# Kernel optimization log

Hardware: AMD Instinct MI355X
Metric: run time of the kernel (lower is better)

Reference implementation:

```python
import jax, jax.numpy as jnp
import numpy as np

HEADS = 8
DIM_HEAD = 64
SCALE = DIM_HEAD ** -0.5


def setup_inputs() -> dict:
    key = jax.random.key(0)
    ks = jax.random.split(key, 6)
    B, N, D = 4, 2048, 512
    inner = HEADS * DIM_HEAD  # 512
    x = jax.random.normal(ks[0], (B, N, D), dtype=jnp.float32)
    centroid_delta = jax.random.normal(ks[1], (B, 3, N, N), dtype=jnp.float32)
    Wqkv = jax.random.normal(ks[2], (D, 3 * inner), dtype=jnp.float32) * (D ** -0.5)
    Wout = jax.random.normal(ks[3], (inner, D), dtype=jnp.float32) * (inner ** -0.5)
    bout = jnp.zeros((D,), dtype=jnp.float32)
    rel_w = jax.random.normal(ks[4], (HEADS, 3), dtype=jnp.float32)
    rel_b = jnp.zeros((HEADS,), dtype=jnp.float32)
    return {"x": x, "centroid_delta": centroid_delta, "Wqkv": Wqkv,
            "Wout": Wout, "bout": bout, "rel_w": rel_w, "rel_b": rel_b}


def reference(x, centroid_delta, Wqkv, Wout, bout, rel_w, rel_b):
    B, N, D = x.shape
    h, d = HEADS, DIM_HEAD
    qkv = x @ Wqkv                      # [B, N, 3*h*d]
    q, k, v = jnp.split(qkv, 3, axis=-1)
    # [B, N, h*d] -> [B, h, N, d]
    reshape = lambda t: t.reshape(B, N, h, d).transpose(0, 2, 1, 3)
    q, k, v = reshape(q), reshape(k), reshape(v)
    dots = jnp.einsum('bhid,bhjd->bhij', q, k) * SCALE  # [B, h, N, N]
    # 1x1 conv: Conv2d(3, heads, 1) on centroid_delta [B, 3, N, N]
    bias = jnp.einsum('hc,bcij->bhij', rel_w, centroid_delta) + rel_b[None, :, None, None]
    attn = jax.nn.softmax(dots + bias, axis=-1)
    out = jnp.einsum('bhij,bhjd->bhid', attn, v)        # [B, h, N, d]
    out = out.transpose(0, 2, 1, 3).reshape(B, N, h * d)
    return out @ Wout + bout
```

## Files before the change

### kernel.cpp

```cpp
#include <hip/hip_runtime.h>
#include <hip/hip_bf16.h>
#include <hip/hip_fp16.h>

typedef __bf16 bf16_t;
typedef __bf16 bf16x8 __attribute__((ext_vector_type(8)));
typedef float f32x4 __attribute__((ext_vector_type(4)));

#define SCALE_ 0.125f
#define BATCH 4
#define NSEQ 2048
#define DMODEL 512
#define HEADS 8
#define DHEAD 64
#define QKVN 1536
#define NN ((size_t)NSEQ * NSEQ)

#define BAR() asm volatile("s_waitcnt lgkmcnt(0)\n\ts_barrier" ::: "memory")

__device__ __forceinline__ void gload_lds16(const void* g, void* l) {
  __builtin_amdgcn_global_load_lds((const __attribute__((address_space(1))) void*)g,
                                   (__attribute__((address_space(3))) void*)l, 16, 0, 0);
}

__device__ __forceinline__ f32x4 mfma16(bf16x8 a, bf16x8 b, f32x4 c) {
  return __builtin_amdgcn_mfma_f32_16x16x32_bf16(a, b, c, 0, 0, 0);
}

__device__ __forceinline__ int pkmax_f16(int a, int b) {
  int d;
  asm("v_pk_max_f16 %0, %1, %2" : "=v"(d) : "v"(a), "v"(b));
  return d;
}

template<int CTRL>
__device__ __forceinline__ int movdpp(int x) {
  return __builtin_amdgcn_update_dpp(0, x, CTRL, 0xf, 0xf, true);
}

__global__ __launch_bounds__(256) void cvt_bf16_kernel(const float* __restrict__ in,
                                                       bf16_t* __restrict__ out, int n4) {
  int i = blockIdx.x * 256 + threadIdx.x;
  if (i < n4) {
    float4 v = ((const float4*)in)[i];
    union { bf16_t b[4]; uint2 u; } pk;
    pk.b[0] = (bf16_t)v.x; pk.b[1] = (bf16_t)v.y;
    pk.b[2] = (bf16_t)v.z; pk.b[3] = (bf16_t)v.w;
    ((uint2*)out)[i] = pk.u;
  }
}

__global__ __launch_bounds__(256) void cvt_transpose_kernel(const float* __restrict__ in,
                                                            bf16_t* __restrict__ out, int R, int C) {
  __shared__ float tile[64][65];
  const int r0 = blockIdx.y * 64, c0 = blockIdx.x * 64;
  const int tx = threadIdx.x & 63, tg = threadIdx.x >> 6;
#pragma unroll
  for (int i = 0; i < 16; i++) {
    int rr = tg * 16 + i;
    tile[rr][tx] = in[(size_t)(r0 + rr) * C + c0 + tx];
  }
  __syncthreads();
#pragma unroll
  for (int i = 0; i < 16; i++) {
    int cc = tg * 16 + i;
    out[(size_t)(c0 + cc) * R + r0 + tx] = (bf16_t)tile[tx][cc];
  }
}

template<int BIAS, int OUTF32, int VSPLIT>
__global__ __launch_bounds__(256) void gemm128_kernel(const bf16_t* __restrict__ A,
    const bf16_t* __restrict__ Bt, void* __restrict__ Cout,
    const float* __restrict__ bias, bf16_t* __restrict__ vt, int M, int N, int K) {
  __shared__ __align__(16) bf16_t SM[2][128 * 64];
  bf16_t* As = SM[0];
  bf16_t* Bs = SM[1];
  const int tid = threadIdx.x;
  const int w = tid >> 6, lane = tid & 63, quad = lane >> 4, l16 = lane & 15;
  const int wm = w & 1, wn = w >> 1;
  const int m0 = blockIdx.x * 128, n0 = blockIdx.y * 128;
  f32x4 acc[4][4] = {};
  int srow[4], scg[4];
#pragma unroll
  for (int t = 0; t < 4; t++) {
    int s = (w * 4 + t) * 64 + lane;
    srow[t] = s >> 3;
    scg[t] = (s & 7) ^ (srow[t] & 7);
  }
  for (int k0 = 0; k0 < K; k0 += 64) {
#pragma unroll
    for (int t = 0; t < 4; t++) {
      gload_lds16(&A[(size_t)(m0 + srow[t]) * K + k0 + scg[t] * 8], &As[(w * 4 + t) * 512]);
      gload_lds16(&Bt[(size_t)(n0 + srow[t]) * K + k0 + scg[t] * 8], &Bs[(w * 4 + t) * 512]);
    }
    __syncthreads();
    bf16x8 af[4][2], bfr[4][2];
#pragma unroll
    for (int mt = 0; mt < 4; mt++) {
      int row = wm * 64 + mt * 16 + l16;
#pragma unroll
      for (int kh = 0; kh < 2; kh++)
        af[mt][kh] = *(const bf16x8*)&As[(row * 8 + ((kh * 4 + quad) ^ (row & 7))) * 8];
    }
#pragma unroll
    for (int nt = 0; nt < 4; nt++) {
      int row = wn * 64 + nt * 16 + l16;
#pragma unroll
      for (int kh = 0; kh < 2; kh++)
        bfr[nt][kh] = *(const bf16x8*)&Bs[(row * 8 + ((kh * 4 + quad) ^ (row & 7))) * 8];
    }
#pragma unroll
    for (int mt = 0; mt < 4; mt++)
#pragma unroll
      for (int nt = 0; nt < 4; nt++) {
        acc[mt][nt] = mfma16(af[mt][0], bfr[nt][0], acc[mt][nt]);
        acc[mt][nt] = mfma16(af[mt][1], bfr[nt][1], acc[mt][nt]);
      }
    __syncthreads();
  }
  if (VSPLIT && n0 >= 1024) {
    bf16_t* T = &SM[0][0];
#pragma unroll
    for (int nt = 0; nt < 4; nt++) {
      int hdl = wn * 64 + nt * 16 + l16;
#pragma unroll
      for (int mt = 0; mt < 4; mt++) {
        int nloc = wm * 64 + mt * 16 + quad * 4;
        union { bf16_t e[4]; uint2 u; } pk;
#pragma unroll
        for (int rr = 0; rr < 4; rr++) pk.e[rr] = (bf16_t)acc[mt][nt][rr];
        *(uint2*)&T[hdl * 128 + nloc] = pk.u;
      }
    }
    __syncthreads();
    const int bb = m0 >> 11, nn0 = m0 & 2047;
#pragma unroll
    for (int pass = 0; pass < 2; pass++) {
      const int r = pass * 64 + (tid >> 2);
      const size_t gb = ((size_t)(bb * 512 + (n0 - 1024) + r)) * NSEQ + nn0;
#pragma unroll
      for (int i = 0; i < 4; i++) {
        int c = i * 32 + (tid & 3) * 8;
        *(uint4*)&vt[gb + c] = *(const uint4*)&T[r * 128 + c];
      }
    }
    return;
  }
#pragma unroll
  for (int nt = 0; nt < 4; nt++) {
    int col = n0 + wn * 64 + nt * 16 + l16;
    float bv = BIAS ? bias[col] : 0.0f;
#pragma unroll
    for (int mt = 0; mt < 4; mt++) {
#pragma unroll
      for (int rr = 0; rr < 4; rr++) {
        int row = m0 + wm * 64 + mt * 16 + quad * 4 + rr;
        float v = acc[mt][nt][rr] + bv;
        if (OUTF32) ((float*)Cout)[(size_t)row * N + col] = v;
        else        ((bf16_t*)Cout)[(size_t)row * N + col] = (bf16_t)v;
      }
    }
  }
}

__global__ __launch_bounds__(256, 4) void attn_kernel(const bf16_t* __restrict__ qkv,
    const bf16_t* __restrict__ vt,
    const float* __restrict__ cd, const float* __restrict__ rel_w,
    const float* __restrict__ rel_b, bf16_t* __restrict__ ao) {
  __shared__ __align__(16) bf16_t Ks[64][72];
  __shared__ __align__(16) bf16_t Vts[64][72];
  __shared__ __align__(16) bf16_t Ps[64][72];
  const int tid = threadIdx.x;
  const int w = tid >> 6, lane = tid & 63, quad = lane >> 4, l16 = lane & 15;
  const int bid = blockIdx.x;
  const int h = bid >> 7, b = (bid >> 5) & 3, it = bid & 31;

  const size_t qoff = (size_t)(b * NSEQ + it * 64 + w * 16 + l16) * QKVN + h * DHEAD;
  bf16x8 q0 = *(const bf16x8*)&qkv[qoff + quad * 8];
  bf16x8 q1 = *(const bf16x8*)&qkv[qoff + 32 + quad * 8];

  const float rw0 = rel_w[h * 3 + 0], rw1 = rel_w[h * 3 + 1], rw2 = rel_w[h * 3 + 2];
  const float rb = rel_b[h];

  bf16x8 ones;
#pragma unroll
  for (int e = 0; e < 8; e++) ones[e] = (bf16_t)1.0f;

  f32x4 o[4] = {};
  float m_r[4], l_r[4];
#pragma unroll
  for (int r = 0; r < 4; r++) { m_r[r] = -1e30f; l_r[r] = 0.0f; }

  const int sr = tid >> 3, sg = tid & 7;
  const size_t kbase = (size_t)b * NSEQ * QKVN + DMODEL + h * DHEAD;
  const size_t vtb = (size_t)(b * HEADS + h) * 64 * NSEQ;
  const int vc0 = (sg ^ ((sr >> 3) & 3)) * 8;

  const int row0 = it * 64 + w * 16 + quad * 4;
  const float* cdp = cd + (size_t)b * 3 * NN + (size_t)row0 * NSEQ + l16;
  float biasr[4][4];
#define LOADBIAS(JT) do { const int jb_ = (JT) * 64;                                   \
  _Pragma("unroll") for (int ct_ = 0; ct_ < 4; ct_++)                                  \
  _Pragma("unroll") for (int r_ = 0; r_ < 4; r_++) {                                   \
    size_t ci_ = (size_t)r_ * NSEQ + jb_ + ct_ * 16;                                   \
    biasr[ct_][r_] = fmaf(rw0, cdp[ci_],                                               \
                     fmaf(rw1, cdp[ci_ + NN], fmaf(rw2, cdp[ci_ + 2 * NN], rb)));      \
  } } while (0)

  uint4 k0r, k1r, v0r, v1r;
  {
    const bf16_t* p = &qkv[kbase + (size_t)sr * QKVN + sg * 8];
    k0r = *(const uint4*)p;
    k1r = *(const uint4*)(p + 32 * QKVN);
    const bf16_t* pv = &vt[vtb + (size_t)sr * NSEQ + sg * 8];
    v0r = *(const uint4*)pv;
    v1r = *(const uint4*)(pv + 32 * NSEQ);
  }
  LOADBIAS(0);

  for (int jt = 0; jt < 32; jt++) {
    *(uint4*)&Ks[sr][sg * 8]      = k0r;
    *(uint4*)&Ks[sr + 32][sg * 8] = k1r;
    *(uint4*)&Vts[sr][vc0]        = v0r;
    *(uint4*)&Vts[sr + 32][vc0]   = v1r;
    BAR();

    if (jt < 31) {
      const bf16_t* p = &qkv[kbase + (size_t)((jt + 1) * 64 + sr) * QKVN + sg * 8];
      k0r = *(const uint4*)p;
      k1r = *(const uint4*)(p + 32 * QKVN);
      const bf16_t* pv = &vt[vtb + (size_t)sr * NSEQ + (jt + 1) * 64 + sg * 8];
      v0r = *(const uint4*)pv;
      v1r = *(const uint4*)(pv + 32 * NSEQ);
    }

    f32x4 s[4] = {};
#pragma unroll
    for (int ct = 0; ct < 4; ct++) {
      bf16x8 b0 = *(const bf16x8*)&Ks[ct * 16 + l16][quad * 8];
      bf16x8 b1 = *(const bf16x8*)&Ks[ct * 16 + l16][32 + quad * 8];
      s[ct] = mfma16(q0, b0, s[ct]);
      s[ct] = mfma16(q1, b1, s[ct]);
    }

#pragma unroll
    for (int ct = 0; ct < 4; ct++)
#pragma unroll
      for (int r = 0; r < 4; r++)
        s[ct][r] = s[ct][r] * SCALE_ + biasr[ct][r];
    if (jt < 31) LOADBIAS(jt + 1);

    float mx[4];
#pragma unroll
    for (int r = 0; r < 4; r++)
      mx[r] = fmaxf(fmaxf(s[0][r], s[1][r]), fmaxf(s[2][r], s[3][r]));
    {
      union { __half h[2]; int i; } u01, u23;
      u01.h[0] = __float2half(mx[0]); u01.h[1] = __float2half(mx[1]);
      u23.h[0] = __float2half(mx[2]); u23.h[1] = __float2half(mx[3]);
      u01.i = pkmax_f16(u01.i, movdpp<0x128>(u01.i));
      u23.i = pkmax_f16(u23.i, movdpp<0x128>(u23.i));
      u01.i = pkmax_f16(u01.i, movdpp<0x124>(u01.i));
      u23.i = pkmax_f16(u23.i, movdpp<0x124>(u23.i));
      u01.i = pkmax_f16(u01.i, movdpp<0x122>(u01.i));
      u23.i = pkmax_f16(u23.i, movdpp<0x122>(u23.i));
      u01.i = pkmax_f16(u01.i, movdpp<0x121>(u01.i));
      u23.i = pkmax_f16(u23.i, movdpp<0x121>(u23.i));
      mx[0] = __half2float(u01.h[0]); mx[1] = __half2float(u01.h[1]);
      mx[2] = __half2float(u23.h[0]); mx[3] = __half2float(u23.h[1]);
    }
    float alpha[4];
#pragma unroll
    for (int r = 0; r < 4; r++) {
      float mnew = fmaxf(m_r[r], mx[r]);
      alpha[r] = __expf(m_r[r] - mnew);
      m_r[r] = mnew;
#pragma unroll
      for (int ct = 0; ct < 4; ct++)
        s[ct][r] = __expf(s[ct][r] - mnew);
#pragma unroll
      for (int dt = 0; dt < 4; dt++) o[dt][r] *= alpha[r];
    }

#pragma unroll
    for (int ct = 0; ct < 4; ct++)
#pragma unroll
      for (int rr = 0; rr < 4; rr++)
        Ps[w * 16 + quad * 4 + rr][(ct * 16 + l16) ^ (quad << 3)] = (bf16_t)s[ct][rr];

    const int psw = ((l16 >> 2) & 3) << 3;
    bf16x8 p0 = *(const bf16x8*)&Ps[w * 16 + l16][(quad * 8) ^ psw];
    bf16x8 p1 = *(const bf16x8*)&Ps[w * 16 + l16][32 + ((quad * 8) ^ psw)];
#pragma unroll
    for (int dt = 0; dt < 4; dt++) {
      const int row = dt * 16 + l16;
      const int vsw = ((row >> 3) & 3) << 3;
      bf16x8 v0 = *(const bf16x8*)&Vts[row][(quad * 8) ^ vsw];
      bf16x8 v1 = *(const bf16x8*)&Vts[row][32 + ((quad * 8) ^ vsw)];
      o[dt] = mfma16(p0, v0, o[dt]);
      o[dt] = mfma16(p1, v1, o[dt]);
    }
    {
      f32x4 ls = {};
      ls = mfma16(p0, ones, ls);
      ls = mfma16(p1, ones, ls);
#pragma unroll
      for (int r = 0; r < 4; r++) l_r[r] = l_r[r] * alpha[r] + ls[r];
    }
    BAR();
  }

#pragma unroll
  for (int dt = 0; dt < 4; dt++) {
    int col = h * DHEAD + dt * 16 + l16;
#pragma unroll
    for (int rr = 0; rr < 4; rr++) {
      int row = b * NSEQ + it * 64 + w * 16 + quad * 4 + rr;
      ao[(size_t)row * DMODEL + col] = (bf16_t)(o[dt][rr] / l_r[rr]);
    }
  }
#undef LOADBIAS
}

extern "C" void kernel_launch(void* const* d_in, const int* in_sizes, int n_in,
                              void* d_out, int out_size, void* d_ws, size_t ws_size,
                              hipStream_t stream) {
  const float* x     = (const float*)d_in[0];
  const float* cd    = (const float*)d_in[1];
  const float* Wqkv  = (const float*)d_in[2];
  const float* Wout  = (const float*)d_in[3];
  const float* bout  = (const float*)d_in[4];
  const float* rel_w = (const float*)d_in[5];
  const float* rel_b = (const float*)d_in[6];
  float* out = (float*)d_out;

  char* ws = (char*)d_ws;
  const size_t M = (size_t)BATCH * NSEQ;
  bf16_t* xb    = (bf16_t*)ws;
  bf16_t* WqkvT = (bf16_t*)(ws + 8388608);
  bf16_t* WoutT = (bf16_t*)(ws + 8388608 + 1572864);
  bf16_t* qkv   = (bf16_t*)(ws + 8388608 + 1572864 + 524288);
  bf16_t* ao    = (bf16_t*)(ws + 8388608 + 1572864 + 524288 + 25165824);
  bf16_t* vtw   = (bf16_t*)(ws + 8388608 + 1572864 + 524288 + 25165824 + 8388608);

  cvt_bf16_kernel<<<(int)(M * DMODEL / 4 / 256), 256, 0, stream>>>(x, xb, (int)(M * DMODEL / 4));
  cvt_transpose_kernel<<<dim3(QKVN / 64, DMODEL / 64), 256, 0, stream>>>(Wqkv, WqkvT, DMODEL, QKVN);
  cvt_transpose_kernel<<<dim3(DMODEL / 64, DMODEL / 64), 256, 0, stream>>>(Wout, WoutT, DMODEL, DMODEL);

  gemm128_kernel<0, 0, 1><<<dim3(M / 128, QKVN / 128), 256, 0, stream>>>(
      xb, WqkvT, (void*)qkv, nullptr, vtw, (int)M, QKVN, DMODEL);

  attn_kernel<<<BATCH * 32 * HEADS, 256, 0, stream>>>(qkv, vtw, cd, rel_w, rel_b, ao);

  gemm128_kernel<1, 1, 0><<<dim3(M / 128, DMODEL / 128), 256, 0, stream>>>(
      ao, WoutT, (void*)out, bout, nullptr, (int)M, DMODEL, DMODEL);
}
```

Before: 454.0 us.

## Split attention over two key halves and merge partial softmax results

Each attention block now processes half of the key sequence, doubling the grid so more blocks run concurrently across compute units. Unnormalized fp32 partial outputs plus per-row max and sum are written to workspace. A new merge kernel combines the two halves with log-sum-exp rescaling and writes bf16 output. This adds extra global traffic for the partials and one more kernel launch.

```diff
diff --git a/kernel.cpp b/kernel.cpp
--- a/kernel.cpp
+++ b/kernel.cpp
@@ -165,14 +165,17 @@
 __global__ __launch_bounds__(256, 4) void attn_kernel(const bf16_t* __restrict__ qkv,
     const bf16_t* __restrict__ vt,
     const float* __restrict__ cd, const float* __restrict__ rel_w,
-    const float* __restrict__ rel_b, bf16_t* __restrict__ ao) {
+    const float* __restrict__ rel_b, float* __restrict__ opart,
+    float2* __restrict__ mls) {
   __shared__ __align__(16) bf16_t Ks[64][72];
   __shared__ __align__(16) bf16_t Vts[64][72];
   __shared__ __align__(16) bf16_t Ps[64][72];
   const int tid = threadIdx.x;
   const int w = tid >> 6, lane = tid & 63, quad = lane >> 4, l16 = lane & 15;
   const int bid = blockIdx.x;
-  const int h = bid >> 7, b = (bid >> 5) & 3, it = bid & 31;
+  const int hj = bid >> 7, h = hj >> 1, jh = hj & 1;
+  const int b = (bid >> 5) & 3, it = bid & 31;
+  const int jbase = jh * 1024;
 
   const size_t qoff = (size_t)(b * NSEQ + it * 64 + w * 16 + l16) * QKVN + h * DHEAD;
   bf16x8 q0 = *(const bf16x8*)&qkv[qoff + quad * 8];
@@ -198,7 +201,7 @@
   const int row0 = it * 64 + w * 16 + quad * 4;
   const float* cdp = cd + (size_t)b * 3 * NN + (size_t)row0 * NSEQ + l16;
   float biasr[4][4];
-#define LOADBIAS(JT) do { const int jb_ = (JT) * 64;                                   \
+#define LOADBIAS(JTA) do { const int jb_ = (JTA) * 64;                                 \
   _Pragma("unroll") for (int ct_ = 0; ct_ < 4; ct_++)                                  \
   _Pragma("unroll") for (int r_ = 0; r_ < 4; r_++) {                                   \
     size_t ci_ = (size_t)r_ * NSEQ + jb_ + ct_ * 16;                                   \
@@ -208,27 +211,27 @@
 
   uint4 k0r, k1r, v0r, v1r;
   {
-    const bf16_t* p = &qkv[kbase + (size_t)sr * QKVN + sg * 8];
+    const bf16_t* p = &qkv[kbase + (size_t)(jbase + sr) * QKVN + sg * 8];
     k0r = *(const uint4*)p;
     k1r = *(const uint4*)(p + 32 * QKVN);
-    const bf16_t* pv = &vt[vtb + (size_t)sr * NSEQ + sg * 8];
+    const bf16_t* pv = &vt[vtb + (size_t)sr * NSEQ + jbase + sg * 8];
     v0r = *(const uint4*)pv;
     v1r = *(const uint4*)(pv + 32 * NSEQ);
   }
-  LOADBIAS(0);
-
-  for (int jt = 0; jt < 32; jt++) {
+  LOADBIAS(jh * 16);
+
+  for (int jt = 0; jt < 16; jt++) {
     *(uint4*)&Ks[sr][sg * 8]      = k0r;
     *(uint4*)&Ks[sr + 32][sg * 8] = k1r;
     *(uint4*)&Vts[sr][vc0]        = v0r;
     *(uint4*)&Vts[sr + 32][vc0]   = v1r;
     BAR();
 
-    if (jt < 31) {
-      const bf16_t* p = &qkv[kbase + (size_t)((jt + 1) * 64 + sr) * QKVN + sg * 8];
+    if (jt < 15) {
+      const bf16_t* p = &qkv[kbase + (size_t)(jbase + (jt + 1) * 64 + sr) * QKVN + sg * 8];
       k0r = *(const uint4*)p;
       k1r = *(const uint4*)(p + 32 * QKVN);
-      const bf16_t* pv = &vt[vtb + (size_t)sr * NSEQ + (jt + 1) * 64 + sg * 8];
+      const bf16_t* pv = &vt[vtb + (size_t)sr * NSEQ + jbase + (jt + 1) * 64 + sg * 8];
       v0r = *(const uint4*)pv;
       v1r = *(const uint4*)(pv + 32 * NSEQ);
     }
@@ -247,7 +250,7 @@
 #pragma unroll
       for (int r = 0; r < 4; r++)
         s[ct][r] = s[ct][r] * SCALE_ + biasr[ct][r];
-    if (jt < 31) LOADBIAS(jt + 1);
+    if (jt < 15) LOADBIAS(jh * 16 + jt + 1);
 
     float mx[4];
 #pragma unroll
@@ -309,16 +312,47 @@
     BAR();
   }
 
+  float* ob = opart + (size_t)bid * 4096;
 #pragma unroll
   for (int dt = 0; dt < 4; dt++) {
-    int col = h * DHEAD + dt * 16 + l16;
+    int col = dt * 16 + l16;
 #pragma unroll
     for (int rr = 0; rr < 4; rr++) {
-      int row = b * NSEQ + it * 64 + w * 16 + quad * 4 + rr;
-      ao[(size_t)row * DMODEL + col] = (bf16_t)(o[dt][rr] / l_r[rr]);
+      int rl = w * 16 + quad * 4 + rr;
+      ob[rl * 64 + col] = o[dt][rr];
+    }
+  }
+  if (l16 == 0) {
+#pragma unroll
+    for (int r = 0; r < 4; r++) {
+      int rl = w * 16 + quad * 4 + r;
+      mls[(size_t)bid * 64 + rl] = make_float2(m_r[r], l_r[r]);
     }
   }
 #undef LOADBIAS
+}
+
+__global__ __launch_bounds__(256) void merge_kernel(const float* __restrict__ opart,
+    const float2* __restrict__ mls, bf16_t* __restrict__ ao) {
+  int qi = blockIdx.x * 256 + threadIdx.x;
+  int gr = qi >> 7;
+  int c4 = (qi & 127) << 2;
+  int h = c4 >> 6, d = c4 & 63;
+  int b = gr >> 11, n = gr & 2047, it = n >> 6, rl = n & 63;
+  int bid0 = h * 256 + b * 32 + it;
+  int bid1 = bid0 + 128;
+  float2 s0 = mls[(size_t)bid0 * 64 + rl];
+  float2 s1 = mls[(size_t)bid1 * 64 + rl];
+  float m = fmaxf(s0.x, s1.x);
+  float e0 = __expf(s0.x - m), e1 = __expf(s1.x - m);
+  float rinv = 1.0f / (s0.y * e0 + s1.y * e1);
+  f32x4 o0 = *(const f32x4*)&opart[(size_t)bid0 * 4096 + rl * 64 + d];
+  f32x4 o1 = *(const f32x4*)&opart[(size_t)bid1 * 4096 + rl * 64 + d];
+  union { bf16_t e[4]; uint2 u; } pk;
+#pragma unroll
+  for (int i = 0; i < 4; i++)
+    pk.e[i] = (bf16_t)((o0[i] * e0 + o1[i] * e1) * rinv);
+  *(uint2*)&ao[(size_t)gr * DMODEL + c4] = pk.u;
 }
 
 extern "C" void kernel_launch(void* const* d_in, const int* in_sizes, int n_in,
@@ -338,9 +372,11 @@
   bf16_t* xb    = (bf16_t*)ws;
   bf16_t* WqkvT = (bf16_t*)(ws + 8388608);
   bf16_t* WoutT = (bf16_t*)(ws + 8388608 + 1572864);
-  bf16_t* qkv   = (bf16_t*)(ws + 8388608 + 1572864 + 524288);
-  bf16_t* ao    = (bf16_t*)(ws + 8388608 + 1572864 + 524288 + 25165824);
-  bf16_t* vtw   = (bf16_t*)(ws + 8388608 + 1572864 + 524288 + 25165824 + 8388608);
+  bf16_t* qkv   = (bf16_t*)(ws + 10485760);
+  bf16_t* ao    = (bf16_t*)(ws + 35651584);
+  bf16_t* vtw   = (bf16_t*)(ws + 44040192);
+  float*  opart = (float*)(ws + 52428800);
+  float2* mls   = (float2*)(ws + 85983232);
 
   cvt_bf16_kernel<<<(int)(M * DMODEL / 4 / 256), 256, 0, stream>>>(x, xb, (int)(M * DMODEL / 4));
   cvt_transpose_kernel<<<dim3(QKVN / 64, DMODEL / 64), 256, 0, stream>>>(Wqkv, WqkvT, DMODEL, QKVN);
@@ -349,7 +385,9 @@
   gemm128_kernel<0, 0, 1><<<dim3(M / 128, QKVN / 128), 256, 0, stream>>>(
       xb, WqkvT, (void*)qkv, nullptr, vtw, (int)M, QKVN, DMODEL);
 
-  attn_kernel<<<BATCH * 32 * HEADS, 256, 0, stream>>>(qkv, vtw, cd, rel_w, rel_b, ao);
+  attn_kernel<<<2048, 256, 0, stream>>>(qkv, vtw, cd, rel_w, rel_b, opart, mls);
+
+  merge_kernel<<<4096, 256, 0, stream>>>(opart, mls, ao);
 
   gemm128_kernel<1, 1, 0><<<dim3(M / 128, DMODEL / 128), 256, 0, stream>>>(
       ao, WoutT, (void*)out, bout, nullptr, (int)M, DMODEL, DMODEL);
```

New measurement: 542.4 us. +19.5%, slower.
